# Kernel optimization log

Measured on AMD Instinct MI355X. Metric: run time of the kernel, lower is better.

## Reference

```python
import jax, jax.numpy as jnp
import numpy as np

MARGIN = 0.0
GAP = 0.4
N, D, C = 8192, 128, 10


def setup_inputs() -> dict:
    key = jax.random.key(0)
    k1, k2, k3 = jax.random.split(key, 3)
    inputs = jax.random.normal(k1, (N, D), dtype=jnp.float32)
    pred = jax.random.normal(k2, (N, C), dtype=jnp.float32)
    targets = jax.random.randint(k3, (N,), 0, C, dtype=jnp.int64)
    return {"inputs": inputs, "pred": pred, "targets": targets}


def reference(inputs, pred, targets):
    n = inputs.shape[0]
    # pairwise euclidean distances: ||xi||^2 + ||xj||^2 - 2 xi.xj, clamped + sqrt
    sq = jnp.sum(inputs * inputs, axis=1)                      # [n]
    dist = sq[:, None] + sq[None, :] - 2.0 * (inputs @ inputs.T)
    dist = jnp.sqrt(jnp.clip(dist, 1e-12))                     # [n, n]
    same = targets[:, None] == targets[None, :]                # [n, n] bool

    # confusion detection (original runs under no_grad)
    p = jax.nn.softmax(jax.lax.stop_gradient(pred), axis=1)
    val, top2 = jax.lax.top_k(p, 2)                            # [n,2]
    confuse = (val[:, 0] - val[:, 1] <= GAP) | (top2[:, 0] != targets)  # [n]

    # hard mining per row: hardest positive (max over same-class), hardest negative (min over diff-class)
    dist_ap = jnp.max(jnp.where(same, dist, -jnp.inf), axis=1)  # [n]
    dist_an = jnp.min(jnp.where(same, jnp.inf, dist), axis=1)   # [n]

    # MarginRankingLoss(margin=MARGIN) with y=1: mean(relu(-(an - ap) + margin)) over confused rows
    per_row = jnp.maximum(dist_ap - dist_an + MARGIN, 0.0)
    cnt = jnp.sum(confuse.astype(jnp.float32))
    loss = jnp.sum(jnp.where(confuse, per_row, 0.0)) / jnp.maximum(cnt, 1.0)
    return jnp.where(cnt > 0, loss, 0.0)
```

## Files before the change

### kernel.cpp

```cpp
#include <hip/hip_runtime.h>

#define NROWS 8192
#define DIMX  128
#define KB    192
#define KSEG  12
#define PTB   24576
#define NKS   3
#define NCLS  10
#define GAPV  0.4f
#define DEBIAS 504.03125f
#define SCL   (-0.0078125f)
#define RGR   256
#define NRG   (NROWS / RGR)
#define CHUNK 256
#define NCHUNK (NROWS / CHUNK)
#define SLAB  64
#define NSLAB (CHUNK / SLAB)

typedef __attribute__((ext_vector_type(4))) int i32x4;

#define GLOAD_LDS16(g, l)                                              \
  __builtin_amdgcn_global_load_lds(                                    \
      (const __attribute__((address_space(1))) void*)(g),              \
      (__attribute__((address_space(3))) void*)(l), 16, 0, 0)

__device__ __forceinline__ int q8(float v) {
  int q = (int)rintf(16.f * v);
  return q > 127 ? 127 : (q < -127 ? -127 : q);
}

__device__ __forceinline__ unsigned ordu(float f) {
  unsigned b = __float_as_uint(f);
  return (b & 0x80000000u) ? ~b : (b | 0x80000000u);
}
__device__ __forceinline__ float deco(unsigned u) {
  return __uint_as_float((u & 0x80000000u) ? (u ^ 0x80000000u) : ~u);
}

__global__ __launch_bounds__(256) void prep_k(const float* __restrict__ x,
                                              const int* __restrict__ tgt,
                                              const float* __restrict__ pred,
                                              char* __restrict__ xa,
                                              char* __restrict__ xbm,
                                              float* __restrict__ sq,
                                              int* __restrict__ conf,
                                              unsigned* __restrict__ umax,
                                              unsigned* __restrict__ umin,
                                              unsigned* __restrict__ ctrs) {
  if (blockIdx.x == 0 && threadIdx.x < 3) ctrs[threadIdx.x] = 0u;
  if (threadIdx.x < 4) {
    const int r = blockIdx.x * 4 + threadIdx.x;
    umax[r] = 0u;
    umin[r] = 0xFFFFFFFFu;
  }

  const int wave = threadIdx.x >> 6;
  const int lane = threadIdx.x & 63;
  const int row  = blockIdx.x * 4 + wave;
  const float2 f2 = ((const float2*)(x + (size_t)row * DIMX))[lane];
  float s = f2.x * f2.x + f2.y * f2.y;
  #pragma unroll
  for (int m = 1; m < 64; m <<= 1) s += __shfl_xor(s, m, 64);

  char* basea = xa  + (size_t)(row >> 7) * PTB + (size_t)(row & 127) * 16;
  char* baseb = xbm + (size_t)(row >> 7) * PTB + (size_t)(row & 127) * 16;
  {
    const int q0 = q8(f2.x), q1 = q8(f2.y);
    const unsigned short u = (unsigned short)((q0 & 0xFF) | ((q1 & 0xFF) << 8));
    const size_t off = (size_t)(lane >> 3) * 2048 + (lane & 7) * 2;
    *(unsigned short*)(basea + off) = u;
    *(unsigned short*)(baseb + off) = u;
  }
  const int cls = tgt[row];
  if (lane < 32) {
    const int j = 2 * lane;
    const int c = j >> 2;
    const bool hit = (c < NCLS) && (c == cls);
    const unsigned short ua = hit ? (unsigned short)0x7F7F : 0;
    const unsigned short ub = hit ? (unsigned short)0x8181 : 0;
    const size_t off = (size_t)(8 + (j >> 4)) * 2048 + (j & 15);
    *(unsigned short*)(basea + off) = ua;
    *(unsigned short*)(baseb + off) = ub;
  }

  if (lane == 0) {
    sq[row] = s;
    const float* pp = pred + (size_t)row * NCLS;
    float v[NCLS];
    #pragma unroll
    for (int c = 0; c < NCLS; ++c) v[c] = pp[c];
    float m1 = v[0]; int i1 = 0;
    #pragma unroll
    for (int c = 1; c < NCLS; ++c)
      if (v[c] > m1) { m1 = v[c]; i1 = c; }
    float m2 = -INFINITY, sum = 0.f;
    #pragma unroll
    for (int c = 0; c < NCLS; ++c) {
      sum += __expf(v[c] - m1);
      if (c != i1) m2 = fmaxf(m2, v[c]);
    }
    const float d01 = (1.f - __expf(m2 - m1)) / sum;
    conf[row] = (d01 <= GAPV) || (i1 != cls);
  }
}

__global__ __launch_bounds__(256)
__attribute__((amdgpu_waves_per_eu(3, 8)))
void gram_k(const char* __restrict__ xa,
            const char* __restrict__ xbm,
            const float* __restrict__ sq,
            unsigned* __restrict__ umax,
            unsigned* __restrict__ umin) {
  __shared__ char  ldsb[2][KSEG * 1024];
  __shared__ float sqb[2][SLAB];
  const int tid  = threadIdx.x;
  const int wave = tid >> 6;
  const int lane = tid & 63;
  const int quad = lane >> 4;
  const int m16  = lane & 15;
  const int bx = blockIdx.x, by = blockIdx.y;

  i32x4 A[4][NKS];
  #pragma unroll
  for (int rt = 0; rt < 4; ++rt) {
    const int rbase = wave * 64 + rt * 16;
    const char* pa = xa + (size_t)(bx * 2 + (rbase >> 7)) * PTB
                        + (size_t)((rbase & 127) + m16) * 16;
    #pragma unroll
    for (int ks = 0; ks < NKS; ++ks)
      A[rt][ks] = *(const i32x4*)(pa + (size_t)(ks * 4 + quad) * 2048);
  }
  #pragma unroll
  for (int rt = 0; rt < 4; ++rt)
    #pragma unroll
    for (int ks = 0; ks < NKS; ++ks)
      asm("" : "+v"(A[rt][ks]));

  float gmin[4][4], gmax[4][4];
  #pragma unroll
  for (int r = 0; r < 4; ++r)
    #pragma unroll
    for (int q = 0; q < 4; ++q) { gmin[r][q] = INFINITY; gmax[r][q] = -INFINITY; }

  {
    const char* srcb = xbm + (size_t)(by * 2) * PTB;
    #pragma unroll
    for (int u = 0; u < 3; ++u) {
      const int kseg = wave * 3 + u;
      GLOAD_LDS16(srcb + (size_t)kseg * 2048 + lane * 16, &ldsb[0][kseg * 1024 + lane * 16]);
    }
    if (wave == 3 && lane < 16)
      GLOAD_LDS16((const char*)(sq + by * CHUNK) + lane * 16, (char*)&sqb[0][0] + lane * 16);
  }

  for (int s = 0; s < NSLAB; ++s) {
    __syncthreads();
    if (s + 1 < NSLAB) {
      const char* srcb = xbm + (size_t)(by * 2 + ((s + 1) >> 1)) * PTB + ((s + 1) & 1) * 1024;
      char* dstb = &ldsb[(s + 1) & 1][0];
      #pragma unroll
      for (int u = 0; u < 3; ++u) {
        const int kseg = wave * 3 + u;
        GLOAD_LDS16(srcb + (size_t)kseg * 2048 + lane * 16, dstb + kseg * 1024 + lane * 16);
      }
      if (wave == 3 && lane < 16)
        GLOAD_LDS16((const char*)(sq + by * CHUNK + (s + 1) * SLAB) + lane * 16,
                    (char*)&sqb[(s + 1) & 1][0] + lane * 16);
    }
    const char* buf = &ldsb[s & 1][0];
    #pragma unroll
    for (int jt = 0; jt < 4; ++jt) {
      i32x4 B[NKS];
      #pragma unroll
      for (int ks = 0; ks < NKS; ++ks)
        B[ks] = *(const i32x4*)(buf + (ks * 4 + quad) * 1024 + (jt * 16 + m16) * 16);
      const float sqj = sqb[s & 1][jt * 16 + m16];

      i32x4 acc[4];
      #pragma unroll
      for (int r = 0; r < 4; ++r) acc[r] = (i32x4){0, 0, 0, 0};
      #pragma unroll
      for (int ks = 0; ks < NKS; ++ks)
        #pragma unroll
        for (int r = 0; r < 4; ++r)
          acc[r] = __builtin_amdgcn_mfma_i32_16x16x64_i8(A[r][ks], B[ks], acc[r], 0, 0, 0);

      #pragma unroll
      for (int r = 0; r < 4; ++r)
        #pragma unroll
        for (int q = 0; q < 4; ++q) {
          const float cand = fmaf((float)acc[r][q], SCL, sqj);
          gmin[r][q] = fminf(gmin[r][q], cand);
          gmax[r][q] = fmaxf(gmax[r][q], cand);
        }
    }
  }

  #pragma unroll
  for (int m = 1; m <= 8; m <<= 1)
    #pragma unroll
    for (int r = 0; r < 4; ++r)
      #pragma unroll
      for (int q = 0; q < 4; ++q) {
        gmin[r][q] = fminf(gmin[r][q], __shfl_xor(gmin[r][q], m, 64));
        gmax[r][q] = fmaxf(gmax[r][q], __shfl_xor(gmax[r][q], m, 64));
      }

  if (m16 == 0) {
    const int rowb = bx * RGR + wave * 64 + quad * 4;
    #pragma unroll
    for (int r = 0; r < 4; ++r)
      #pragma unroll
      for (int q = 0; q < 4; ++q) {
        atomicMax(&umax[rowb + r * 16 + q], ordu(gmax[r][q]));
        atomicMin(&umin[rowb + r * 16 + q], ordu(gmin[r][q]));
      }
  }
}

__global__ __launch_bounds__(256) void reduce_k(const unsigned* __restrict__ umax,
                                                const unsigned* __restrict__ umin,
                                                const float* __restrict__ sq,
                                                const int* __restrict__ conf,
                                                unsigned* __restrict__ ctrs,
                                                float* __restrict__ out) {
  __shared__ float red[2][4];
  const int tid = threadIdx.x, bx = blockIdx.x;
  const int wave = tid >> 6, lane = tid & 63;
  const int row = bx * RGR + tid;

  unsigned* g_done = ctrs;
  float*    Ssum   = (float*)(ctrs + 1);
  float*    Csum   = (float*)(ctrs + 2);

  const float hi = deco(umax[row]);
  const float lo = deco(umin[row]);
  float ps = 0.f, pc = 0.f;
  if (conf[row]) {
    const float ap = sqrtf(fmaxf(sq[row] + hi - DEBIAS, 1e-12f));
    const float an = sqrtf(fmaxf(sq[row] + lo, 1e-12f));
    ps = fmaxf(ap - an, 0.f);
    pc = 1.f;
  }
  #pragma unroll
  for (int m = 1; m < 64; m <<= 1) {
    ps += __shfl_xor(ps, m, 64);
    pc += __shfl_xor(pc, m, 64);
  }
  if (lane == 0) { red[0][wave] = ps; red[1][wave] = pc; }
  __syncthreads();
  if (tid == 0) {
    atomicAdd(Ssum, red[0][0] + red[0][1] + red[0][2] + red[0][3]);
    atomicAdd(Csum, red[1][0] + red[1][1] + red[1][2] + red[1][3]);
    __threadfence();
    if (atomicAdd(g_done, 1u) == NRG - 1u) {
      const float St = atomicAdd(Ssum, 0.f);
      const float Ct = atomicAdd(Csum, 0.f);
      out[0] = (Ct > 0.f) ? (St / fmaxf(Ct, 1.f)) : 0.f;
    }
  }
}

extern "C" void kernel_launch(void* const* d_in, const int* in_sizes, int n_in,
                              void* d_out, int out_size, void* d_ws, size_t ws_size,
                              hipStream_t stream) {
  const float* x    = (const float*)d_in[0];
  const float* pred = (const float*)d_in[1];
  const int*   tgt  = (const int*)d_in[2];
  float* out = (float*)d_out;

  char* w = (char*)d_ws;
  const size_t arr_bytes = (size_t)NROWS * KB;
  char*     xa   = w;
  char*     xbm  = w + arr_bytes;
  float*    sq   = (float*)(w + 2 * arr_bytes);
  int*      conf = (int*)(w + 2 * arr_bytes + (size_t)NROWS * 4);
  unsigned* umax = (unsigned*)(w + 2 * arr_bytes + (size_t)NROWS * 8);
  unsigned* umin = (unsigned*)(w + 2 * arr_bytes + (size_t)NROWS * 12);
  unsigned* ctrs = (unsigned*)(w + 2 * arr_bytes + (size_t)NROWS * 16);

  hipLaunchKernelGGL(prep_k, dim3(NROWS / 4), dim3(256), 0, stream,
                     x, tgt, pred, xa, xbm, sq, conf, umax, umin, ctrs);
  hipLaunchKernelGGL(gram_k, dim3(NRG, NCHUNK), dim3(256), 0, stream,
                     xa, xbm, sq, umax, umin);
  hipLaunchKernelGGL(reduce_k, dim3(NRG), dim3(256), 0, stream,
                     umax, umin, sq, conf, ctrs, out);
}
```

Baseline: 88.23 us.

## Load B tiles directly into registers with prefetch, drop LDS staging

The gram kernel no longer stages B fragments through double-buffered LDS with global_load_lds and per-slab barriers. Each wave now loads its B fragments and squared norms straight from global memory into registers, prefetching the next 16-column tile while computing the current one. The column chunk per block doubles to 512, which halves the grid in y and amortizes the A-register loads over more columns. The trade-off is that all four waves redundantly fetch the same B data from L2/L1 instead of sharing it via LDS, and there are fewer blocks to fill the device.

```diff
diff --git a/kernel.cpp b/kernel.cpp
--- a/kernel.cpp
+++ b/kernel.cpp
@@ -12,17 +12,11 @@
 #define SCL   (-0.0078125f)
 #define RGR   256
 #define NRG   (NROWS / RGR)
-#define CHUNK 256
+#define CHUNK 512
 #define NCHUNK (NROWS / CHUNK)
-#define SLAB  64
-#define NSLAB (CHUNK / SLAB)
+#define NT    (CHUNK / 16)
 
 typedef __attribute__((ext_vector_type(4))) int i32x4;
-
-#define GLOAD_LDS16(g, l)                                              \
-  __builtin_amdgcn_global_load_lds(                                    \
-      (const __attribute__((address_space(1))) void*)(g),              \
-      (__attribute__((address_space(3))) void*)(l), 16, 0, 0)
 
 __device__ __forceinline__ int q8(float v) {
   int q = (int)rintf(16.f * v);
@@ -111,8 +105,6 @@
             const float* __restrict__ sq,
             unsigned* __restrict__ umax,
             unsigned* __restrict__ umin) {
-  __shared__ char  ldsb[2][KSEG * 1024];
-  __shared__ float sqb[2][SLAB];
   const int tid  = threadIdx.x;
   const int wave = tid >> 6;
   const int lane = tid & 63;
@@ -142,39 +134,25 @@
     #pragma unroll
     for (int q = 0; q < 4; ++q) { gmin[r][q] = INFINITY; gmax[r][q] = -INFINITY; }
 
-  {
-    const char* srcb = xbm + (size_t)(by * 2) * PTB;
-    #pragma unroll
-    for (int u = 0; u < 3; ++u) {
-      const int kseg = wave * 3 + u;
-      GLOAD_LDS16(srcb + (size_t)kseg * 2048 + lane * 16, &ldsb[0][kseg * 1024 + lane * 16]);
-    }
-    if (wave == 3 && lane < 16)
-      GLOAD_LDS16((const char*)(sq + by * CHUNK) + lane * 16, (char*)&sqb[0][0] + lane * 16);
-  }
-
-  for (int s = 0; s < NSLAB; ++s) {
-    __syncthreads();
-    if (s + 1 < NSLAB) {
-      const char* srcb = xbm + (size_t)(by * 2 + ((s + 1) >> 1)) * PTB + ((s + 1) & 1) * 1024;
-      char* dstb = &ldsb[(s + 1) & 1][0];
-      #pragma unroll
-      for (int u = 0; u < 3; ++u) {
-        const int kseg = wave * 3 + u;
-        GLOAD_LDS16(srcb + (size_t)kseg * 2048 + lane * 16, dstb + kseg * 1024 + lane * 16);
-      }
-      if (wave == 3 && lane < 16)
-        GLOAD_LDS16((const char*)(sq + by * CHUNK + (s + 1) * SLAB) + lane * 16,
-                    (char*)&sqb[(s + 1) & 1][0] + lane * 16);
-    }
-    const char* buf = &ldsb[s & 1][0];
+  const char*  bl  = xbm + (size_t)(by * 4) * PTB + (size_t)m16 * 16 + (size_t)quad * 2048;
+  const float* sqp = sq + by * CHUNK + m16;
+
+  i32x4 Bc[NKS], Bn[NKS];
+  float sqc, sqn;
+  #pragma unroll
+  for (int ks = 0; ks < NKS; ++ks) Bc[ks] = *(const i32x4*)(bl + ks * 8192);
+  sqc = sqp[0];
+
+  for (int s = 0; s < NT / 4; ++s) {
     #pragma unroll
     for (int jt = 0; jt < 4; ++jt) {
-      i32x4 B[NKS];
+      const int u  = s * 4 + jt;
+      const int un = (u + 1 < NT) ? u + 1 : NT - 1;
+      const size_t toff = (size_t)(un >> 3) * PTB + (size_t)(un & 7) * 256;
       #pragma unroll
       for (int ks = 0; ks < NKS; ++ks)
-        B[ks] = *(const i32x4*)(buf + (ks * 4 + quad) * 1024 + (jt * 16 + m16) * 16);
-      const float sqj = sqb[s & 1][jt * 16 + m16];
+        Bn[ks] = *(const i32x4*)(bl + toff + ks * 8192);
+      sqn = sqp[un * 16];
 
       i32x4 acc[4];
       #pragma unroll
@@ -183,16 +161,20 @@
       for (int ks = 0; ks < NKS; ++ks)
         #pragma unroll
         for (int r = 0; r < 4; ++r)
-          acc[r] = __builtin_amdgcn_mfma_i32_16x16x64_i8(A[r][ks], B[ks], acc[r], 0, 0, 0);
+          acc[r] = __builtin_amdgcn_mfma_i32_16x16x64_i8(A[r][ks], Bc[ks], acc[r], 0, 0, 0);
 
       #pragma unroll
       for (int r = 0; r < 4; ++r)
         #pragma unroll
         for (int q = 0; q < 4; ++q) {
-          const float cand = fmaf((float)acc[r][q], SCL, sqj);
+          const float cand = fmaf((float)acc[r][q], SCL, sqc);
           gmin[r][q] = fminf(gmin[r][q], cand);
           gmax[r][q] = fmaxf(gmax[r][q], cand);
         }
+
+      #pragma unroll
+      for (int ks = 0; ks < NKS; ++ks) Bc[ks] = Bn[ks];
+      sqc = sqn;
     }
   }
 
```

After: 86.15 us. 1.02x faster.
